# Kernel tuning notes

Hardware: AMD Instinct MI355X
Metric: run time of the kernel (lower is better)

The kernel has to match this reference:

```python
import jax, jax.numpy as jnp
import numpy as np

S, K, O = 8192, 1024, 4096  # seq_len, in_features, out_features


def setup_inputs() -> dict:
    key = jax.random.key(0)
    k1, k2, k3, k4, k5 = jax.random.split(key, 5)
    x = jax.random.randint(k1, (S, K), -128, 128, dtype=jnp.int8)
    weight_q = jax.random.randint(k2, (O, K), -128, 128, dtype=jnp.int8)
    scale_x = jax.random.uniform(k3, (), jnp.float32, 0.01, 0.1)
    scale_w = jax.random.uniform(k4, (), jnp.float32, 0.01, 0.1)
    scale_y = jax.random.uniform(k5, (S,), jnp.float32, 0.5, 2.0)  # per-row output scale
    return {"x": x, "weight_q": weight_q, "scale_x": scale_x,
            "scale_w": scale_w, "scale_y": scale_y}


def reference(x, weight_q, scale_x, scale_w, scale_y):
    # int8 GEMM with int32 accumulation: [S,K] @ [O,K]^T -> [S,O]
    acc = jnp.einsum('sk,ok->so', x.astype(jnp.int32), weight_q.astype(jnp.int32))
    # fused per-row requantization: scale_y[:seq_len] gives per-row scale
    requant_scale = (scale_x * scale_w / scale_y).astype(jnp.float32)  # [S]
    scaled = acc.astype(jnp.float32) * requant_scale[:, None]
    out_q = jnp.clip(jnp.round(scaled), -128.0, 127.0).astype(jnp.int8)
    return out_q, scale_y
```

## Files before the change

### kernel.cpp

```cpp
#include <hip/hip_runtime.h>


#define S_DIM 8192
#define K_DIM 1024
#define O_DIM 4096
#define BM 256
#define BN 128
#define BK 64
#define NITER (K_DIM / BK)
#define TILE_BYTES (128 * BK)
#define A_SLOT (2 * TILE_BYTES)
#define B_SLOT TILE_BYTES

using i32x4 = __attribute__((ext_vector_type(4))) int;

__device__ __forceinline__ void load_lds16(const void* g, void* l) {
  __builtin_amdgcn_global_load_lds(
      (const __attribute__((address_space(1))) void*)g,
      (__attribute__((address_space(3))) void*)l, 16, 0, 0);
}

__global__ void pack_kernel(const int* __restrict__ xi, const int* __restrict__ wi,
                            const float* __restrict__ sy,
                            uint4* __restrict__ ap, uint4* __restrict__ bp,
                            float* __restrict__ out_sy) {
  const int tid = blockIdx.x * blockDim.x + threadIdx.x;
  const int nA = S_DIM * K_DIM / 16;
  const int nB = O_DIM * K_DIM / 16;

  const int* src;
  uint4* dst;
  int j;
  if (tid < nA) {
    src = xi; dst = ap; j = tid;
  } else if (tid < nA + nB) {
    src = wi; dst = bp; j = tid - nA;
  } else {
    return;
  }
  const int t = j >> 9;
  const int idx = j & 511;
  const int r = idx >> 2;
  const int cs = idx & 3;
  const int c = cs ^ (r & 3);
  const int band = t >> 4;
  const int kt = t & 15;
  const int row = band * 128 + r;
  const int4* s4 = (const int4*)src + row * 256 + kt * 16 + c * 4;
  int4 v0 = s4[0], v1 = s4[1], v2 = s4[2], v3 = s4[3];
  uint4 o;
  o.x = (v0.x & 0xff) | ((v0.y & 0xff) << 8) | ((v0.z & 0xff) << 16) | (((unsigned)v0.w & 0xff) << 24);
  o.y = (v1.x & 0xff) | ((v1.y & 0xff) << 8) | ((v1.z & 0xff) << 16) | (((unsigned)v1.w & 0xff) << 24);
  o.z = (v2.x & 0xff) | ((v2.y & 0xff) << 8) | ((v2.z & 0xff) << 16) | (((unsigned)v2.w & 0xff) << 24);
  o.w = (v3.x & 0xff) | ((v3.y & 0xff) << 8) | ((v3.z & 0xff) << 16) | (((unsigned)v3.w & 0xff) << 24);
  dst[j] = o;
  if (tid < S_DIM) out_sy[tid] = sy[tid];
}

__global__ __launch_bounds__(512, 4) void gemm_i8_kernel(
    const signed char* __restrict__ Ap,
    const signed char* __restrict__ Bp,
    const float* __restrict__ sx, const float* __restrict__ sw,
    const float* __restrict__ sy, float* __restrict__ out) {
  __shared__ __align__(16) signed char As[3][A_SLOT];
  __shared__ __align__(16) signed char Bs[3][B_SLOT];

  const int tid = threadIdx.x;
  const int wave = tid >> 6;
  const int lane = tid & 63;
  const int wm = wave >> 1;
  const int wn = wave & 1;
  const int rowBase = blockIdx.x * BM;
  const int colBase = blockIdx.y * BN;

  const int soff = wave * 1024 + lane * 16;
  const signed char* gA0 = Ap + (size_t)(2 * blockIdx.x) * NITER * TILE_BYTES + soff;
  const signed char* gA1 = Ap + (size_t)(2 * blockIdx.x + 1) * NITER * TILE_BYTES + soff;
  const signed char* gB  = Bp + (size_t)blockIdx.y * NITER * TILE_BYTES + soff;
  signed char* ldsA = (signed char*)As + soff;
  signed char* ldsB = (signed char*)Bs + soff;

  i32x4 acc[4][4] = {};

  const int fr = lane & 15;
  const int fq = (((lane >> 4) ^ (fr & 3)) & 3) * 16;

  load_lds16(gA0, ldsA);
  load_lds16(gA1, ldsA + TILE_BYTES);
  load_lds16(gB, ldsB);
  asm volatile("" ::: "memory");
  {
    const size_t goff = TILE_BYTES;
    load_lds16(gA0 + goff, ldsA + A_SLOT);
    load_lds16(gA1 + goff, ldsA + A_SLOT + TILE_BYTES);
    load_lds16(gB + goff, ldsB + B_SLOT);
  }

#pragma unroll
  for (int it = 0; it < NITER; ++it) {
    if (it + 1 < NITER) {
      asm volatile("s_waitcnt vmcnt(3) lgkmcnt(0)" ::: "memory");
    } else {
      asm volatile("s_waitcnt vmcnt(0) lgkmcnt(0)" ::: "memory");
    }
    __builtin_amdgcn_s_barrier();
    asm volatile("" ::: "memory");

    if (it + 2 < NITER) {
      const int slot = (it + 2) % 3;
      const size_t goff = (size_t)(it + 2) * TILE_BYTES;
      load_lds16(gA0 + goff, ldsA + slot * A_SLOT);
      load_lds16(gA1 + goff, ldsA + slot * A_SLOT + TILE_BYTES);
      load_lds16(gB + goff, ldsB + slot * B_SLOT);
    }

    const signed char* curA = As[it % 3];
    const signed char* curB = Bs[it % 3];
    i32x4 bf[4];
#pragma unroll
    for (int ni = 0; ni < 4; ++ni)
      bf[ni] = *(const i32x4*)(curB + (wn * 64 + ni * 16 + fr) * BK + fq);

#pragma unroll
    for (int mi = 0; mi < 4; ++mi) {
      i32x4 af = *(const i32x4*)(curA + (wm * 64 + mi * 16 + fr) * BK + fq);
#pragma unroll
      for (int ni = 0; ni < 4; ++ni)
        acc[mi][ni] =
            __builtin_amdgcn_mfma_i32_16x16x64_i8(af, bf[ni], acc[mi][ni], 0, 0, 0);
    }
  }

  const float sxw = sx[0] * sw[0];
  const int quad = lane >> 4;
#pragma unroll
  for (int mi = 0; mi < 4; ++mi) {
#pragma unroll
    for (int r = 0; r < 4; ++r) {
      const int s = rowBase + wm * 64 + mi * 16 + quad * 4 + r;
      const float rs = sxw / sy[s];
      float* orow = out + (size_t)s * O_DIM + colBase + wn * 64 + fr;
#pragma unroll
      for (int ni = 0; ni < 4; ++ni) {
        float f = rintf((float)acc[mi][ni][r] * rs);
        f = fminf(127.0f, fmaxf(-128.0f, f));
        orow[ni * 16] = f;
      }
    }
  }
}

extern "C" void kernel_launch(void* const* d_in, const int* in_sizes, int n_in,
                              void* d_out, int out_size, void* d_ws, size_t ws_size,
                              hipStream_t stream) {
  const int* x = (const int*)d_in[0];
  const int* w = (const int*)d_in[1];
  const float* sx = (const float*)d_in[2];
  const float* sw = (const float*)d_in[3];
  const float* sy = (const float*)d_in[4];
  float* out = (float*)d_out;

  uint4* ap = (uint4*)d_ws;
  uint4* bp = ap + (size_t)S_DIM * K_DIM / 16;

  const int total = S_DIM * K_DIM / 16 + O_DIM * K_DIM / 16;
  pack_kernel<<<(total + 255) / 256, 256, 0, stream>>>(
      x, w, sy, ap, bp, out + (size_t)S_DIM * O_DIM);

  dim3 grid(S_DIM / BM, O_DIM / BN);
  gemm_i8_kernel<<<grid, 512, 0, stream>>>(
      (const signed char*)ap, (const signed char*)bp, sx, sw, sy, out);
}
```

Baseline: 199.6 us.

## Enlarge GEMM tile to 256x256 with interleaved prefetch and MFMA priority phases

Widens the block tile from 256x128 to 256x256, so each wave computes a 128x64 sub-tile with 8x4 accumulators and reuses each loaded B fragment across twice as many MFMAs. Global-to-LDS prefetches are spread across four sub-phases of each K step, and every phase is bracketed by barriers with raised wave priority around the MFMA burst. The aim is to raise arithmetic intensity and overlap memory with compute, at the cost of higher register and LDS use, occupancy lowered to 2 blocks per CU, and a grid half as large.

Result: slower. 212.3 us (+6.4%).

```diff
diff --git a/kernel.cpp b/kernel.cpp
--- a/kernel.cpp
+++ b/kernel.cpp
@@ -5,12 +5,13 @@
 #define K_DIM 1024
 #define O_DIM 4096
 #define BM 256
-#define BN 128
+#define BN 256
 #define BK 64
 #define NITER (K_DIM / BK)
 #define TILE_BYTES (128 * BK)
+#define BAND_BYTES (NITER * TILE_BYTES)
 #define A_SLOT (2 * TILE_BYTES)
-#define B_SLOT TILE_BYTES
+#define B_SLOT (2 * TILE_BYTES)
 
 using i32x4 = __attribute__((ext_vector_type(4))) int;
 
@@ -19,6 +20,9 @@
       (const __attribute__((address_space(1))) void*)g,
       (__attribute__((address_space(3))) void*)l, 16, 0, 0);
 }
+
+#define FENCE() asm volatile("" ::: "memory")
+#define BARRIER() asm volatile("s_barrier" ::: "memory")
 
 __global__ void pack_kernel(const int* __restrict__ xi, const int* __restrict__ wi,
                             const float* __restrict__ sy,
@@ -57,7 +61,7 @@
   if (tid < S_DIM) out_sy[tid] = sy[tid];
 }
 
-__global__ __launch_bounds__(512, 4) void gemm_i8_kernel(
+__global__ __launch_bounds__(512, 2) void gemm_i8_kernel(
     const signed char* __restrict__ Ap,
     const signed char* __restrict__ Bp,
     const float* __restrict__ sx, const float* __restrict__ sw,
@@ -68,76 +72,91 @@
   const int tid = threadIdx.x;
   const int wave = tid >> 6;
   const int lane = tid & 63;
-  const int wm = wave >> 1;
-  const int wn = wave & 1;
+  const int wm = wave >> 2;
+  const int wn = wave & 3;
   const int rowBase = blockIdx.x * BM;
   const int colBase = blockIdx.y * BN;
 
   const int soff = wave * 1024 + lane * 16;
-  const signed char* gA0 = Ap + (size_t)(2 * blockIdx.x) * NITER * TILE_BYTES + soff;
-  const signed char* gA1 = Ap + (size_t)(2 * blockIdx.x + 1) * NITER * TILE_BYTES + soff;
-  const signed char* gB  = Bp + (size_t)blockIdx.y * NITER * TILE_BYTES + soff;
+  const signed char* gA0 = Ap + (size_t)(2 * blockIdx.x) * BAND_BYTES + soff;
+  const signed char* gA1 = Ap + (size_t)(2 * blockIdx.x + 1) * BAND_BYTES + soff;
+  const signed char* gB0 = Bp + (size_t)(2 * blockIdx.y) * BAND_BYTES + soff;
+  const signed char* gB1 = Bp + (size_t)(2 * blockIdx.y + 1) * BAND_BYTES + soff;
   signed char* ldsA = (signed char*)As + soff;
   signed char* ldsB = (signed char*)Bs + soff;
 
-  i32x4 acc[4][4] = {};
+  i32x4 acc[8][4] = {};
 
   const int fr = lane & 15;
   const int fq = (((lane >> 4) ^ (fr & 3)) & 3) * 16;
 
+  const int aoff = wm * TILE_BYTES + fr * 64 + fq;
+  const int boff = (wn >> 1) * TILE_BYTES + ((wn & 1) * 64 + fr) * 64 + fq;
+
   load_lds16(gA0, ldsA);
   load_lds16(gA1, ldsA + TILE_BYTES);
-  load_lds16(gB, ldsB);
-  asm volatile("" ::: "memory");
-  {
-    const size_t goff = TILE_BYTES;
-    load_lds16(gA0 + goff, ldsA + A_SLOT);
-    load_lds16(gA1 + goff, ldsA + A_SLOT + TILE_BYTES);
-    load_lds16(gB + goff, ldsB + B_SLOT);
-  }
+  load_lds16(gB0, ldsB);
+  load_lds16(gB1, ldsB + TILE_BYTES);
+  FENCE();
+  load_lds16(gA0 + TILE_BYTES, ldsA + A_SLOT);
+  load_lds16(gA1 + TILE_BYTES, ldsA + A_SLOT + TILE_BYTES);
+  load_lds16(gB0 + TILE_BYTES, ldsB + B_SLOT);
+  load_lds16(gB1 + TILE_BYTES, ldsB + B_SLOT + TILE_BYTES);
 
 #pragma unroll
   for (int it = 0; it < NITER; ++it) {
     if (it + 1 < NITER) {
-      asm volatile("s_waitcnt vmcnt(3) lgkmcnt(0)" ::: "memory");
+      asm volatile("s_waitcnt vmcnt(4) lgkmcnt(0)" ::: "memory");
     } else {
       asm volatile("s_waitcnt vmcnt(0) lgkmcnt(0)" ::: "memory");
     }
-    __builtin_amdgcn_s_barrier();
-    asm volatile("" ::: "memory");
+    BARRIER();
 
-    if (it + 2 < NITER) {
-      const int slot = (it + 2) % 3;
-      const size_t goff = (size_t)(it + 2) * TILE_BYTES;
-      load_lds16(gA0 + goff, ldsA + slot * A_SLOT);
-      load_lds16(gA1 + goff, ldsA + slot * A_SLOT + TILE_BYTES);
-      load_lds16(gB + goff, ldsB + slot * B_SLOT);
-    }
+    const signed char* curA = As[it % 3] + aoff;
+    const signed char* curB = Bs[it % 3] + boff;
+    const int pslot = (it + 2) % 3;
+    const size_t pgoff = (size_t)(it + 2) * TILE_BYTES;
+    const bool pf = (it + 2) < NITER;
 
-    const signed char* curA = As[it % 3];
-    const signed char* curB = Bs[it % 3];
     i32x4 bf[4];
 #pragma unroll
-    for (int ni = 0; ni < 4; ++ni)
-      bf[ni] = *(const i32x4*)(curB + (wn * 64 + ni * 16 + fr) * BK + fq);
+    for (int p = 0; p < 4; ++p) {
+      if (p == 0) {
+#pragma unroll
+        for (int ni = 0; ni < 4; ++ni)
+          bf[ni] = *(const i32x4*)(curB + ni * 1024);
+      }
+      i32x4 af0 = *(const i32x4*)(curA + (2 * p) * 1024);
+      i32x4 af1 = *(const i32x4*)(curA + (2 * p + 1) * 1024);
 
+      if (pf) {
+        if (p == 0) load_lds16(gA0 + pgoff, ldsA + pslot * A_SLOT);
+        if (p == 1) load_lds16(gA1 + pgoff, ldsA + pslot * A_SLOT + TILE_BYTES);
+        if (p == 2) load_lds16(gB0 + pgoff, ldsB + pslot * B_SLOT);
+        if (p == 3) load_lds16(gB1 + pgoff, ldsB + pslot * B_SLOT + TILE_BYTES);
+      }
+
+      BARRIER();
+      __builtin_amdgcn_s_setprio(1);
 #pragma unroll
-    for (int mi = 0; mi < 4; ++mi) {
-      i32x4 af = *(const i32x4*)(curA + (wm * 64 + mi * 16 + fr) * BK + fq);
-#pragma unroll
-      for (int ni = 0; ni < 4; ++ni)
-        acc[mi][ni] =
-            __builtin_amdgcn_mfma_i32_16x16x64_i8(af, bf[ni], acc[mi][ni], 0, 0, 0);
+      for (int ni = 0; ni < 4; ++ni) {
+        acc[2 * p][ni] =
+            __builtin_amdgcn_mfma_i32_16x16x64_i8(af0, bf[ni], acc[2 * p][ni], 0, 0, 0);
+        acc[2 * p + 1][ni] =
+            __builtin_amdgcn_mfma_i32_16x16x64_i8(af1, bf[ni], acc[2 * p + 1][ni], 0, 0, 0);
+      }
+      __builtin_amdgcn_s_setprio(0);
+      BARRIER();
     }
   }
 
   const float sxw = sx[0] * sw[0];
   const int quad = lane >> 4;
 #pragma unroll
-  for (int mi = 0; mi < 4; ++mi) {
+  for (int mi = 0; mi < 8; ++mi) {
 #pragma unroll
     for (int r = 0; r < 4; ++r) {
-      const int s = rowBase + wm * 64 + mi * 16 + quad * 4 + r;
+      const int s = rowBase + wm * 128 + mi * 16 + quad * 4 + r;
       const float rs = sxw / sy[s];
       float* orow = out + (size_t)s * O_DIM + colBase + wn * 64 + fr;
 #pragma unroll
```
